# Optimization experiments

Hardware: AMD Instinct MI355X
Metric: run time of the kernel (lower is better)

Reference implementation:

```python
import jax, jax.numpy as jnp
import numpy as np

N_HEAD = 16
HEAD_SIZE = 64  # n_embd // n_head = 1024 // 16


def setup_inputs() -> dict:
    key = jax.random.key(0)
    k1, k2 = jax.random.split(key)
    B, T, C = 2, 2048, 1024
    x = jax.random.normal(k1, (B, T, C), dtype=jnp.float32)
    w_attn = jax.random.normal(k2, (C, 3 * C), dtype=jnp.float32) * (C ** -0.5)
    b_attn = jnp.zeros((3 * C,), dtype=jnp.float32)
    return {"x": x, "w_attn": w_attn, "b_attn": b_attn}


def reference(x, w_attn, b_attn):
    B, T, C = x.shape
    qkv = x @ w_attn + b_attn  # [B, T, 3C]
    q, k, v = jnp.split(qkv, 3, axis=-1)
    # [B, T, H, D] -> [B, H, T, D]
    def heads(t):
        return t.reshape(B, T, N_HEAD, HEAD_SIZE).transpose(0, 2, 1, 3)
    q, k, v = heads(q), heads(k), heads(v)
    scale = HEAD_SIZE ** -0.5
    wei = jnp.einsum('bhqd,bhkd->bhqk', q, k) * scale  # [B, H, T, T]
    causal = jnp.tril(jnp.ones((T, T), dtype=bool))
    wei = jnp.where(causal, wei, -jnp.inf)
    wei = jax.nn.softmax(wei, axis=-1)
    out = jnp.einsum('bhqk,bhkd->bhqd', wei, v)  # [B, H, T, D]
    out = out.transpose(0, 2, 1, 3).reshape(B, T, C)
    return out
```

## Files before the change

kernel.cpp:

```cpp
#include <hip/hip_runtime.h>
#include <hip/hip_bf16.h>

#define BSZ 2
#define SEQ 2048
#define CDIM 1024
#define NHEAD 16
#define HDIM 64
#define M_GEMM (BSZ * SEQ)
#define N_GEMM (3 * CDIM)
#define K_GEMM CDIM
#define QK_PITCH (2 * CDIM)

typedef __attribute__((ext_vector_type(8))) short short8;
typedef __attribute__((ext_vector_type(4))) short short4v;
typedef __attribute__((ext_vector_type(4))) float f32x4;

__device__ __forceinline__ short bf16_rn(float f) {
    unsigned u = __builtin_bit_cast(unsigned, f);
    u += 0x7FFF + ((u >> 16) & 1);
    return (short)(u >> 16);
}

__device__ __forceinline__ void gl2lds16(const short* g, short* l) {
    __builtin_amdgcn_global_load_lds(
        (const __attribute__((address_space(1))) unsigned int*)g,
        (__attribute__((address_space(3))) unsigned int*)l, 16, 0, 0);
}

#define WAITV4() asm volatile("s_waitcnt vmcnt(4)")
#define WAITV0() asm volatile("s_waitcnt vmcnt(0)")
#define LGKM0()  asm volatile("s_waitcnt lgkmcnt(0)")
#define SCB()    __builtin_amdgcn_sched_barrier(0)
#define BARRIER() __builtin_amdgcn_s_barrier()

__global__ __launch_bounds__(256) void cvt_fused(const float* __restrict__ X,
                                                 const float* __restrict__ W,
                                                 short* __restrict__ Xb,
                                                 short* __restrict__ WT) {
    const int tid = threadIdx.x;
    if (blockIdx.x < 2048) {
        size_t idx = ((size_t)blockIdx.x * 256 + tid) * 8;
        float4 a = *(const float4*)&X[idx];
        float4 b = *(const float4*)&X[idx + 4];
        short8 o;
        o[0] = bf16_rn(a.x); o[1] = bf16_rn(a.y); o[2] = bf16_rn(a.z); o[3] = bf16_rn(a.w);
        o[4] = bf16_rn(b.x); o[5] = bf16_rn(b.y); o[6] = bf16_rn(b.z); o[7] = bf16_rn(b.w);
        *(short8*)&Xb[idx] = o;
        return;
    }
    __shared__ short T[64][72];
    const int bid = blockIdx.x - 2048;
    const int n0 = (bid % 48) * 64;
    const int k0 = (bid / 48) * 64;
#pragma unroll
    for (int pass = 0; pass < 4; ++pass) {
        int i = pass * 256 + tid;
        int kr = i >> 4;
        int n4 = i & 15;
        float4 v = *(const float4*)&W[(size_t)(k0 + kr) * N_GEMM + n0 + n4 * 4];
        T[n4 * 4 + 0][kr] = bf16_rn(v.x);
        T[n4 * 4 + 1][kr] = bf16_rn(v.y);
        T[n4 * 4 + 2][kr] = bf16_rn(v.z);
        T[n4 * 4 + 3][kr] = bf16_rn(v.w);
    }
    __syncthreads();
#pragma unroll
    for (int pass = 0; pass < 2; ++pass) {
        int o = pass * 256 + tid;
        int nr = o >> 3;
        int c8 = o & 7;
        *(short8*)&WT[(size_t)(n0 + nr) * K_GEMM + k0 + c8 * 8] =
            *(const short8*)&T[nr][c8 * 8];
    }
}

#define MFMA_QUAD(MB, NB)                                                     \
    do {                                                                      \
        __builtin_amdgcn_s_setprio(1);                                        \
        _Pragma("unroll")                                                     \
        for (int mi_ = 0; mi_ < 4; ++mi_)                                     \
            _Pragma("unroll")                                                 \
            for (int ni_ = 0; ni_ < 2; ++ni_)                                 \
                _Pragma("unroll")                                             \
                for (int ks_ = 0; ks_ < 2; ++ks_)                             \
                    acc[(MB) + mi_][(NB) + ni_] =                             \
                        __builtin_amdgcn_mfma_f32_16x16x32_bf16(              \
                            Af[mi_][ks_], Bf[(NB) + ni_][ks_],                \
                            acc[(MB) + mi_][(NB) + ni_], 0, 0, 0);            \
        __builtin_amdgcn_s_setprio(0);                                        \
    } while (0)

__global__ __launch_bounds__(512, 2) void qkv_gemm_8ph(const short* __restrict__ A,
                                                       const short* __restrict__ Bt,
                                                       const float* __restrict__ bias,
                                                       short* __restrict__ Yqk,
                                                       short* __restrict__ Yv) {
    __shared__ short Asl[32768];
    __shared__ short Bsl[32768];

    const int tid  = threadIdx.x;
    const int w    = tid >> 6;
    const int lane = tid & 63;
    const int l16  = lane & 15;
    const int quad = lane >> 4;
    const int wm   = w >> 2;
    const int wn   = w & 3;
    const int ls   = lane >> 3;
    const int lc   = lane & 7;
    const int fsw  = l16 & 7;

    const int orig = blockIdx.y * 12 + blockIdx.x;
    const int xcd  = orig & 7;
    const int idx  = orig >> 3;
    const int bM   = ((xcd & 1) << 3) + (idx & 7);
    const int bN   = (xcd >> 1) * 3 + (idx >> 3);
    const int m0   = bM << 8;
    const int n0   = bN << 8;

    const short* Ab = A  + (size_t)m0 * K_GEMM;
    const short* Bb = Bt + (size_t)n0 * K_GEMM;

    f32x4 acc[8][4];
#pragma unroll
    for (int i = 0; i < 8; ++i)
#pragma unroll
        for (int j = 0; j < 4; ++j) acc[i][j] = (f32x4){0.f, 0.f, 0.f, 0.f};

    auto stageA = [&](int unit, int tt, int sbuf) {
#pragma unroll
        for (int i = 0; i < 2; ++i) {
            const int u0 = (i * 8 + w) * 8;
            const int tr = (u0 & 63) + ((u0 >> 6) << 7) + unit * 64;
            gl2lds16(Ab + (size_t)(tr + ls) * K_GEMM + tt * 64 + ((lc ^ ls) << 3),
                     &Asl[sbuf * 16384 + tr * 64]);
        }
    };
    auto stageB = [&](int unit, int tt, int sbuf) {
#pragma unroll
        for (int i = 0; i < 2; ++i) {
            const int u0 = (i * 8 + w) * 8;
            const int tr = (u0 & 31) + ((u0 >> 5) << 6) + unit * 32;
            gl2lds16(Bb + (size_t)(tr + ls) * K_GEMM + tt * 64 + ((lc ^ ls) << 3),
                     &Bsl[sbuf * 16384 + tr * 64]);
        }
    };
    auto rdA = [&](int ab, int mi, int ks) -> short8 {
        const int r = wm * 128 + mi * 16 + l16;
        return *(const short8*)&Asl[ab + r * 64 + ((ks * 4 + quad) ^ fsw) * 8];
    };
    auto rdB = [&](int ab, int ni, int ks) -> short8 {
        const int r = wn * 64 + ni * 16 + l16;
        return *(const short8*)&Bsl[ab + r * 64 + ((ks * 4 + quad) ^ fsw) * 8];
    };

    stageA(0, 0, 0);
    stageB(0, 0, 0);
    stageB(1, 0, 0);
    stageA(1, 0, 0);
    WAITV4();
    SCB();
    BARRIER();
    SCB();

    for (int t = 0; t < 16; ++t) {
        const int buf = t & 1;
        const int sb  = buf ^ 1;
        const int tn  = (t + 1) & 15;
        const int ab  = buf * 16384;

        short8 Af[4][2], Bf[4][2];

#pragma unroll
        for (int mi = 0; mi < 4; ++mi)
#pragma unroll
            for (int ks = 0; ks < 2; ++ks) Af[mi][ks] = rdA(ab, mi, ks);
#pragma unroll
        for (int ni = 0; ni < 2; ++ni)
#pragma unroll
            for (int ks = 0; ks < 2; ++ks) Bf[ni][ks] = rdB(ab, ni, ks);
        stageA(0, tn, sb);
        SCB(); BARRIER(); LGKM0(); SCB();
        MFMA_QUAD(0, 0);
        WAITV4();
        SCB(); BARRIER(); SCB();

#pragma unroll
        for (int ni = 2; ni < 4; ++ni)
#pragma unroll
            for (int ks = 0; ks < 2; ++ks) Bf[ni][ks] = rdB(ab, ni, ks);
        stageB(0, tn, sb);
        SCB(); BARRIER(); LGKM0(); SCB();
        MFMA_QUAD(0, 2);
        WAITV4();
        SCB(); BARRIER(); SCB();

#pragma unroll
        for (int mi = 0; mi < 4; ++mi)
#pragma unroll
            for (int ks = 0; ks < 2; ++ks) Af[mi][ks] = rdA(ab, 4 + mi, ks);
        stageB(1, tn, sb);
        SCB(); BARRIER(); LGKM0(); SCB();
        MFMA_QUAD(4, 0);
        SCB(); BARRIER(); SCB();

        stageA(1, tn, sb);
        SCB(); BARRIER(); SCB();
        MFMA_QUAD(4, 2);
        WAITV4();
        SCB(); BARRIER(); SCB();
    }
    WAITV0();

    if (n0 >= 2 * CDIM) {
#pragma unroll
        for (int mi = 0; mi < 8; ++mi) {
            int row0 = m0 + wm * 128 + mi * 16 + quad * 4;
#pragma unroll
            for (int ni = 0; ni < 4; ++ni) {
                int colg = n0 + wn * 64 + ni * 16 + l16;
                float bb = bias[colg];
                short4v pk;
#pragma unroll
                for (int r = 0; r < 4; ++r) pk[r] = bf16_rn(acc[mi][ni][r] + bb);
                *(short4v*)&Yv[(size_t)(colg - 2 * CDIM) * M_GEMM + row0] = pk;
            }
        }
    } else {
        const float qs = (n0 < CDIM) ? 0.125f * 1.44269504f : 1.0f;
#pragma unroll
        for (int mi = 0; mi < 8; ++mi)
#pragma unroll
            for (int r = 0; r < 4; ++r) {
                int row = m0 + wm * 128 + mi * 16 + quad * 4 + r;
#pragma unroll
                for (int ni = 0; ni < 4; ++ni) {
                    int colg = n0 + wn * 64 + ni * 16 + l16;
                    Yqk[(size_t)row * QK_PITCH + colg] =
                        bf16_rn((acc[mi][ni][r] + bias[colg]) * qs);
                }
            }
    }
}

__global__ __launch_bounds__(256) void attn_mfma(const short* __restrict__ qk,
                                                 const short* __restrict__ vT,
                                                 float* __restrict__ out) {
    const int b = blockIdx.z;
    const int h = blockIdx.y;
    const int bx = blockIdx.x;
    const int u = h + 16 * b;
    const int band = u >> 3;
    const int base = (band & 2) ? ((bx + 16) & 31) : bx;
    const int qt = (band & 1) ? (31 - base) : base;
    const int tid = threadIdx.x;
    const int w = tid >> 6;
    const int lane = tid & 63;
    const int quad = lane >> 4;
    const int l16 = lane & 15;
    const int q0 = qt * 64;

    __shared__ short Ks[2][64 * 64];
    __shared__ short Vt[2][64 * 64];
    __shared__ short Ps[4 * 16 * 64];

    int koff[2], voff[2], ldso[2];
#pragma unroll
    for (int p = 0; p < 2; ++p) {
        int cid = p * 256 + w * 64 + lane;
        int row = cid >> 3;
        int c = (cid & 7) ^ (row & 7);
        koff[p] = row * QK_PITCH + c * 8;
        voff[p] = row * M_GEMM + c * 8;
        ldso[p] = (p * 256 + w * 64) * 8;
    }

    const short* qrow = qk + (size_t)(b * SEQ + q0 + w * 16 + l16) * QK_PITCH + h * HDIM;
    short8 aq[2];
    aq[0] = *(const short8*)(qrow + quad * 8);
    aq[1] = *(const short8*)(qrow + 32 + quad * 8);

    float l_run[4] = {0.f, 0.f, 0.f, 0.f};
    f32x4 o_acc[4];
#pragma unroll
    for (int dt = 0; dt < 4; ++dt) o_acc[dt] = (f32x4){0.f, 0.f, 0.f, 0.f};

    const int rowg0 = q0 + w * 16 + quad * 4;
    const short* kb0 = qk + (size_t)(b * SEQ) * QK_PITCH + CDIM + h * HDIM;
    const short* vb0 = vT + (size_t)(h * HDIM) * M_GEMM + b * SEQ;

    const int ksl = l16 & 7;
    short* PsW = &Ps[w * 1024];

#pragma unroll
    for (int p = 0; p < 2; ++p) {
        gl2lds16(kb0 + koff[p], &Ks[0][ldso[p]]);
        gl2lds16(vb0 + voff[p], &Vt[0][ldso[p]]);
    }
    __syncthreads();

    for (int kt = 0; kt <= qt; ++kt) {
        const int cur = kt & 1;

        if (kt < qt) {
            const short* kbase = kb0 + (size_t)(kt + 1) * 64 * QK_PITCH;
            const short* vbase = vb0 + (kt + 1) * 64;
#pragma unroll
            for (int p = 0; p < 2; ++p) {
                gl2lds16(kbase + koff[p], &Ks[cur ^ 1][ldso[p]]);
                gl2lds16(vbase + voff[p], &Vt[cur ^ 1][ldso[p]]);
            }
        }

        const short* KsC = Ks[cur];
        const short* VtC = Vt[cur];

        f32x4 s[4];
#pragma unroll
        for (int nt = 0; nt < 4; ++nt) s[nt] = (f32x4){0.f, 0.f, 0.f, 0.f};
#pragma unroll
        for (int nt = 0; nt < 4; ++nt)
#pragma unroll
            for (int ks = 0; ks < 2; ++ks) {
                short8 bk = *(const short8*)&KsC[(nt * 16 + l16) * 64 +
                                                 ((ks * 4 + quad) ^ ksl) * 8];
                s[nt] = __builtin_amdgcn_mfma_f32_16x16x32_bf16(aq[ks], bk, s[nt], 0, 0, 0);
            }

        if (kt < qt) {
#pragma unroll
            for (int r = 0; r < 4; ++r) {
                const int qr = quad * 4 + r;
                float lsum = 0.f;
#pragma unroll
                for (int nt = 0; nt < 4; ++nt) {
                    float pp = __builtin_amdgcn_exp2f(s[nt][r]);
                    lsum += pp;
                    int slot = (nt * 2 + (l16 >> 3)) ^ (qr & 7);
                    PsW[qr * 64 + slot * 8 + (l16 & 7)] = bf16_rn(pp);
                }
                l_run[r] += lsum;
            }
        } else {
            const int keyb = kt * 64 + l16;
#pragma unroll
            for (int r = 0; r < 4; ++r) {
                const int qr = quad * 4 + r;
                const int rowg = rowg0 + r;
                float lsum = 0.f;
#pragma unroll
                for (int nt = 0; nt < 4; ++nt) {
                    float pp = __builtin_amdgcn_exp2f(s[nt][r]);
                    pp = ((keyb + nt * 16) > rowg) ? 0.f : pp;
                    lsum += pp;
                    int slot = (nt * 2 + (l16 >> 3)) ^ (qr & 7);
                    PsW[qr * 64 + slot * 8 + (l16 & 7)] = bf16_rn(pp);
                }
                l_run[r] += lsum;
            }
        }

#pragma unroll
        for (int dt = 0; dt < 4; ++dt)
#pragma unroll
            for (int ks = 0; ks < 2; ++ks) {
                short8 ap = *(const short8*)&PsW[l16 * 64 + ((ks * 4 + quad) ^ ksl) * 8];
                short8 bv = *(const short8*)&VtC[(dt * 16 + l16) * 64 +
                                                 ((ks * 4 + quad) ^ ksl) * 8];
                o_acc[dt] = __builtin_amdgcn_mfma_f32_16x16x32_bf16(ap, bv, o_acc[dt], 0, 0, 0);
            }

        __syncthreads();
    }

#pragma unroll
    for (int r = 0; r < 4; ++r) {
        float l = l_run[r];
#pragma unroll
        for (int off = 1; off < 16; off <<= 1)
            l += __shfl_xor(l, off);
        float inv = 1.f / l;
        int row = q0 + w * 16 + quad * 4 + r;
        float* optr = out + (size_t)(b * SEQ + row) * CDIM + h * HDIM;
#pragma unroll
        for (int dt = 0; dt < 4; ++dt)
            optr[dt * 16 + l16] = o_acc[dt][r] * inv;
    }
}

extern "C" void kernel_launch(void* const* d_in, const int* in_sizes, int n_in,
                              void* d_out, int out_size, void* d_ws, size_t ws_size,
                              hipStream_t stream) {
    const float* x      = (const float*)d_in[0];
    const float* w_attn = (const float*)d_in[1];
    const float* b_attn = (const float*)d_in[2];
    float* out = (float*)d_out;

    short* qk  = (short*)d_ws;
    short* vT  = (short*)((char*)d_ws + 16777216);
    short* xb  = (short*)((char*)d_ws + 25165824);
    short* wT  = (short*)((char*)d_ws + 33554432);

    cvt_fused<<<2048 + 768, 256, 0, stream>>>(x, w_attn, xb, wT);

    dim3 g1(N_GEMM / 256, M_GEMM / 256);
    qkv_gemm_8ph<<<g1, 512, 0, stream>>>(xb, wT, b_attn, qk, vT);

    dim3 g2(SEQ / 64, NHEAD, BSZ);
    attn_mfma<<<g2, 256, 0, stream>>>(qk, vT, out);
}
```

Measured before the change: 158.0 us.

## Compute transposed S so P stays in registers, dropping the LDS round-trip

The QK^T MFMA now swaps operands so each lane holds a column of S^T for its own query, which lets the bf16 probabilities be packed straight into the A-operand registers of the PV MFMA. This drops the per-warp Ps shared buffer and its writes and reads. The K tile uses a new swizzle with a permuted key ordering so the register layout matches V's rows, and the row-sum reduction is changed to match. s_setprio calls are added around the MFMA blocks. The risk is that the key permutation or masking index is wrong, and that the different LDS access pattern causes bank conflicts.

```diff
diff --git a/kernel.cpp b/kernel.cpp
--- a/kernel.cpp
+++ b/kernel.cpp
@@ -261,16 +261,17 @@
 
     __shared__ short Ks[2][64 * 64];
     __shared__ short Vt[2][64 * 64];
-    __shared__ short Ps[4 * 16 * 64];
 
     int koff[2], voff[2], ldso[2];
 #pragma unroll
     for (int p = 0; p < 2; ++p) {
         int cid = p * 256 + w * 64 + lane;
         int row = cid >> 3;
-        int c = (cid & 7) ^ (row & 7);
-        koff[p] = row * QK_PITCH + c * 8;
-        voff[p] = row * M_GEMM + c * 8;
+        int hK = (row & 7) ^ (((row >> 4) & 1) << 2) ^ ((row >> 3) & 1);
+        int cK = (cid & 7) ^ hK;
+        int cV = (cid & 7) ^ (row & 7);
+        koff[p] = row * QK_PITCH + cK * 8;
+        voff[p] = row * M_GEMM + cV * 8;
         ldso[p] = (p * 256 + w * 64) * 8;
     }
 
@@ -279,17 +280,18 @@
     aq[0] = *(const short8*)(qrow + quad * 8);
     aq[1] = *(const short8*)(qrow + 32 + quad * 8);
 
-    float l_run[4] = {0.f, 0.f, 0.f, 0.f};
+    float l_run = 0.f;
     f32x4 o_acc[4];
 #pragma unroll
     for (int dt = 0; dt < 4; ++dt) o_acc[dt] = (f32x4){0.f, 0.f, 0.f, 0.f};
 
-    const int rowg0 = q0 + w * 16 + quad * 4;
+    const int qglob = q0 + w * 16 + l16;
     const short* kb0 = qk + (size_t)(b * SEQ) * QK_PITCH + CDIM + h * HDIM;
     const short* vb0 = vT + (size_t)(h * HDIM) * M_GEMM + b * SEQ;
 
     const int ksl = l16 & 7;
-    short* PsW = &Ps[w * 1024];
+
+    const int Fq = ((l16 >> 2) << 3) + (l16 & 3);
 
 #pragma unroll
     for (int p = 0; p < 2; ++p) {
@@ -317,68 +319,70 @@
         f32x4 s[4];
 #pragma unroll
         for (int nt = 0; nt < 4; ++nt) s[nt] = (f32x4){0.f, 0.f, 0.f, 0.f};
-#pragma unroll
-        for (int nt = 0; nt < 4; ++nt)
+        __builtin_amdgcn_s_setprio(1);
+#pragma unroll
+        for (int nt = 0; nt < 4; ++nt) {
+            const int F  = (nt >> 1) * 32 + (nt & 1) * 4 + Fq;
+            const int hF = (F & 7) ^ (((F >> 4) & 1) << 2) ^ ((F >> 3) & 1);
 #pragma unroll
             for (int ks = 0; ks < 2; ++ks) {
-                short8 bk = *(const short8*)&KsC[(nt * 16 + l16) * 64 +
-                                                 ((ks * 4 + quad) ^ ksl) * 8];
-                s[nt] = __builtin_amdgcn_mfma_f32_16x16x32_bf16(aq[ks], bk, s[nt], 0, 0, 0);
+                short8 kf = *(const short8*)&KsC[F * 64 + (((ks * 4 + quad) ^ hF) * 8)];
+                s[nt] = __builtin_amdgcn_mfma_f32_16x16x32_bf16(kf, aq[ks], s[nt], 0, 0, 0);
             }
-
+        }
+        __builtin_amdgcn_s_setprio(0);
+
+        short8 pa0, pa1;
+        float lsum = 0.f;
         if (kt < qt) {
 #pragma unroll
-            for (int r = 0; r < 4; ++r) {
-                const int qr = quad * 4 + r;
-                float lsum = 0.f;
-#pragma unroll
-                for (int nt = 0; nt < 4; ++nt) {
+            for (int nt = 0; nt < 4; ++nt)
+#pragma unroll
+                for (int r = 0; r < 4; ++r) {
                     float pp = __builtin_amdgcn_exp2f(s[nt][r]);
                     lsum += pp;
-                    int slot = (nt * 2 + (l16 >> 3)) ^ (qr & 7);
-                    PsW[qr * 64 + slot * 8 + (l16 & 7)] = bf16_rn(pp);
+                    short pb = bf16_rn(pp);
+                    if (nt < 2) pa0[(nt & 1) * 4 + r] = pb;
+                    else        pa1[(nt & 1) * 4 + r] = pb;
                 }
-                l_run[r] += lsum;
-            }
         } else {
-            const int keyb = kt * 64 + l16;
-#pragma unroll
-            for (int r = 0; r < 4; ++r) {
-                const int qr = quad * 4 + r;
-                const int rowg = rowg0 + r;
-                float lsum = 0.f;
-#pragma unroll
-                for (int nt = 0; nt < 4; ++nt) {
+#pragma unroll
+            for (int nt = 0; nt < 4; ++nt)
+#pragma unroll
+                for (int r = 0; r < 4; ++r) {
+                    int key = kt * 64 + (nt >> 1) * 32 + quad * 8 + (nt & 1) * 4 + r;
                     float pp = __builtin_amdgcn_exp2f(s[nt][r]);
-                    pp = ((keyb + nt * 16) > rowg) ? 0.f : pp;
+                    pp = (key > qglob) ? 0.f : pp;
                     lsum += pp;
-                    int slot = (nt * 2 + (l16 >> 3)) ^ (qr & 7);
-                    PsW[qr * 64 + slot * 8 + (l16 & 7)] = bf16_rn(pp);
+                    short pb = bf16_rn(pp);
+                    if (nt < 2) pa0[(nt & 1) * 4 + r] = pb;
+                    else        pa1[(nt & 1) * 4 + r] = pb;
                 }
-                l_run[r] += lsum;
-            }
-        }
-
+        }
+        l_run += lsum;
+
+        __builtin_amdgcn_s_setprio(1);
 #pragma unroll
         for (int dt = 0; dt < 4; ++dt)
 #pragma unroll
             for (int ks = 0; ks < 2; ++ks) {
-                short8 ap = *(const short8*)&PsW[l16 * 64 + ((ks * 4 + quad) ^ ksl) * 8];
                 short8 bv = *(const short8*)&VtC[(dt * 16 + l16) * 64 +
                                                  ((ks * 4 + quad) ^ ksl) * 8];
-                o_acc[dt] = __builtin_amdgcn_mfma_f32_16x16x32_bf16(ap, bv, o_acc[dt], 0, 0, 0);
+                o_acc[dt] = __builtin_amdgcn_mfma_f32_16x16x32_bf16(
+                    ks ? pa1 : pa0, bv, o_acc[dt], 0, 0, 0);
             }
+        __builtin_amdgcn_s_setprio(0);
 
         __syncthreads();
     }
 
+    float l = l_run;
+    l += __shfl_xor(l, 16);
+    l += __shfl_xor(l, 32);
 #pragma unroll
     for (int r = 0; r < 4; ++r) {
-        float l = l_run[r];
-#pragma unroll
-        for (int off = 1; off < 16; off <<= 1)
-            l += __shfl_xor(l, off);
-        float inv = 1.f / l;
+        float lq = __shfl(l, quad * 4 + r);
+        float inv = 1.f / lq;
         int row = q0 + w * 16 + quad * 4 + r;
         float* optr = out + (size_t)(b * SEQ + row) * CDIM + h * HDIM;
 #pragma unroll
```

Result: faster. 154.7 us (-2.1%).
